# Kernel tuning notes

Measured on AMD Instinct MI355X. Metric: run time of the kernel, lower is better.

## Reference

```python
import jax, jax.numpy as jnp
import numpy as np
import math

EPS = 1e-5  # BatchNorm eps; eval mode with running_mean=0, running_var=1


def maxpool(x, k, p):
    return jax.lax.reduce_window(x, -jnp.inf, jax.lax.max,
                                 (1, 1, k, k), (1, 1, 1, 1),
                                 ((0, 0), (0, 0), (p, p), (p, p)))


def conv1x1(x, w, b=None):
    # x: [B,Cin,H,W], w: [Cout,Cin]
    y = jnp.einsum('oi,bihw->bohw', w, x)
    if b is not None:
        y = y + b[None, :, None, None]
    return y


def bn_eval(x, g, b):
    scale = g / jnp.sqrt(1.0 + EPS)
    return x * scale[None, :, None, None] + b[None, :, None, None]


def setup_inputs() -> dict:
    B, C, H, W = 2, 64, 80, 80
    c1, c2, c3 = 21, 21, 22
    ch = 32  # C//2
    ks = jax.random.split(jax.random.key(0), 16)
    s = 0.05
    inp = {
        'x': jax.random.normal(ks[0], (B, C, H, W), jnp.float32),
        'q1_w': jax.random.normal(ks[1], (c1, c1), jnp.float32) * s,
        'q1_g': jnp.ones((c1,), jnp.float32),
        'q1_b': jnp.zeros((c1,), jnp.float32),
        'q2_w': jax.random.normal(ks[2], (c2, c2), jnp.float32) * s,
        'q2_g': jnp.ones((c2,), jnp.float32),
        'q2_b': jnp.zeros((c2,), jnp.float32),
        'q3_w': jax.random.normal(ks[3], (c3, c3), jnp.float32) * s,
        'q3_g': jnp.ones((c3,), jnp.float32),
        'q3_b': jnp.zeros((c3,), jnp.float32),
        'k_hf_w': jax.random.normal(ks[4], (ch, C), jnp.float32) * s,
        'k_hf_b': jnp.zeros((ch,), jnp.float32),
        'k_lf_w': jax.random.normal(ks[5], (C - ch, C), jnp.float32) * s,
        'k_lf_b': jnp.zeros((C - ch,), jnp.float32),
        'k_fuse_w': jax.random.normal(ks[6], (C, C), jnp.float32) * s,
        'k_fuse_b': jnp.zeros((C,), jnp.float32),
        'v_bn_g': jnp.ones((C,), jnp.float32),
        'v_bn_b': jnp.zeros((C,), jnp.float32),
        'v_w': jax.random.normal(ks[7], (C, C), jnp.float32) * s,
        'v_b': jnp.zeros((C,), jnp.float32),
        'out_w': jax.random.normal(ks[8], (C, C), jnp.float32) * s,
        'out_b': jnp.zeros((C,), jnp.float32),
    }
    return inp


def reference(x, q1_w, q1_g, q1_b, q2_w, q2_g, q2_b, q3_w, q3_g, q3_b,
              k_hf_w, k_hf_b, k_lf_w, k_lf_b, k_fuse_w, k_fuse_b,
              v_bn_g, v_bn_b, v_w, v_b, out_w, out_b):
    B, C, H, W = x.shape
    N = H * W
    c1 = q1_w.shape[0]
    c2 = q2_w.shape[0]
    # Q: ThreeGroupConvQ (split -> 1x1 conv (no bias) -> BN -> ReLU -> concat)
    x1, x2, x3 = jnp.split(x, [c1, c1 + c2], axis=1)
    y1 = jax.nn.relu(bn_eval(conv1x1(x1, q1_w), q1_g, q1_b))
    y2 = jax.nn.relu(bn_eval(conv1x1(x2, q2_w), q2_g, q2_b))
    y3 = jax.nn.relu(bn_eval(conv1x1(x3, q3_w), q3_g, q3_b))
    Q = jnp.concatenate([y1, y2, y3], axis=1)
    # K: ThermalStructureExtractor
    p3 = maxpool(x, 3, 1)
    p5 = maxpool(x, 5, 2)
    low = (p3 + p5) * 0.5
    high = conv1x1(x - low, k_hf_w, k_hf_b)
    lowp = conv1x1(low, k_lf_w, k_lf_b)
    K = conv1x1(jnp.concatenate([high, lowp], axis=1), k_fuse_w, k_fuse_b)
    # V: BN -> 1x1 conv
    V = conv1x1(bn_eval(x, v_bn_g, v_bn_b), v_w, v_b)
    # attention over N = H*W spatial tokens, channel features
    Qc = Q.reshape(B, C, N)
    Kc = K.reshape(B, C, N)
    Vc = V.reshape(B, C, N)
    attn = jax.nn.softmax(
        jnp.einsum('bcn,bcm->bnm', Qc, Kc) / math.sqrt(C), axis=-1)  # [B,N,N]
    out = jnp.einsum('bnm,bcm->bcn', attn, Vc).reshape(B, C, H, W)
    return conv1x1(out, out_w, out_b) + x
```

## Files before the change

### kernel.cpp

```cpp
#include <hip/hip_runtime.h>
#include <hip/hip_bf16.h>


#define BATCH 2
#define CH 64
#define HH 80
#define WW 80
#define NN 6400
#define NT 100
#define KS 5
#define KTPS (NT/KS)
#define EPSV 1e-5f
#define NEGBIG (-1e30f)
#define QP 72
#define LOG2E8 0.18033688f
#define VSP 65

typedef __hip_bfloat16 bf16;
typedef __attribute__((ext_vector_type(8))) short short8;
typedef __attribute__((ext_vector_type(4))) float f4;
#define MFMA16 __builtin_amdgcn_mfma_f32_16x16x32_bf16

__device__ __forceinline__ float b2f(bf16 v){ return __bfloat162float(v); }
__device__ __forceinline__ bf16 f2b(float v){ return __float2bfloat16(v); }
__device__ __forceinline__ float fexp2(float x){
#if __has_builtin(__builtin_amdgcn_exp2f)
  return __builtin_amdgcn_exp2f(x);
#else
  return exp2f(x);
#endif
}

#define OFF_BIAS 0
#define OFF_WH_B 768
#define OFF_LOW_B (768 + 32768)
#define OFF_Q_B   (OFF_LOW_B + BATCH*CH*NN*2)
#define OFF_K_B   (OFF_Q_B   + BATCH*CH*NN*2)
#define OFF_V_B   (OFF_K_B   + BATCH*CH*NN*2)
#define OFF_P_B   (OFF_V_B   + BATCH*CH*NN*2)
#define OFF_ML_B  (OFF_P_B   + BATCH*NT*KS*4096*4)

__global__ __launch_bounds__(256) void setup_fold(
    const float* __restrict__ q1w, const float* __restrict__ q1g, const float* __restrict__ q1b,
    const float* __restrict__ q2w, const float* __restrict__ q2g, const float* __restrict__ q2b,
    const float* __restrict__ q3w, const float* __restrict__ q3g, const float* __restrict__ q3b,
    const float* __restrict__ khw, const float* __restrict__ khb,
    const float* __restrict__ klw, const float* __restrict__ klb,
    const float* __restrict__ kfw, const float* __restrict__ kfb,
    const float* __restrict__ vg,  const float* __restrict__ vbnb,
    const float* __restrict__ vw,  const float* __restrict__ vb,
    float* __restrict__ biasf, bf16* __restrict__ wh)
{
  __shared__ __align__(16) float skf[4096];
  __shared__ __align__(16) float skh[2048];
  __shared__ __align__(16) float skl[2048];

  int tid = threadIdx.x;
  int blk = blockIdx.x;
  #pragma unroll
  for (int i = 0; i < 4; ++i)
    *(float4*)&skf[(i*256 + tid)*4] = *(const float4*)&kfw[(i*256 + tid)*4];
  #pragma unroll
  for (int i = 0; i < 2; ++i) {
    *(float4*)&skh[(i*256 + tid)*4] = *(const float4*)&khw[(i*256 + tid)*4];
    *(float4*)&skl[(i*256 + tid)*4] = *(const float4*)&klw[(i*256 + tid)*4];
  }
  __syncthreads();

  float rs = rsqrtf(1.0f + EPSV);
  bf16* wq   = wh;
  bf16* wvh  = wh + 4096;
  bf16* wa1  = wh + 8192;
  bf16* wa2m = wh + 12288;

  int t = blk*256 + tid;
  int ci = t & 63, co = t >> 6;
  int o = ci*64 + co;

  float w = 0.f, g;
  if (co < 21)      { g = q1g[co];    w = (ci < 21)              ? q1w[co*21 + ci]            : 0.f; }
  else if (co < 42) { g = q2g[co-21]; w = (ci >= 21 && ci < 42)  ? q2w[(co-21)*21 + (ci-21)]  : 0.f; }
  else              { g = q3g[co-42]; w = (ci >= 42)             ? q3w[(co-42)*22 + (ci-42)]  : 0.f; }
  wq[o] = f2b(w * g * rs * LOG2E8);

  float a1 = 0.f, a2 = 0.f;
  #pragma unroll
  for (int j = 0; j < 32; ++j) {
    a1 += skf[co*64 + j]      * skh[j*64 + ci];
    a2 += skf[co*64 + 32 + j] * skl[j*64 + ci];
  }
  wa1[o]  = f2b(a1);
  wa2m[o] = f2b(a2 - a1);
  wvh[o]  = f2b(vw[co*64 + ci] * vg[ci] * rs);

  if (blk == 0 && tid < 64) {
    int c2 = tid;
    float bq;
    if (c2 < 21)      bq = q1b[c2];
    else if (c2 < 42) bq = q2b[c2-21];
    else              bq = q3b[c2-42];
    biasf[c2] = bq * LOG2E8;
    float bk = kfb[c2];
    #pragma unroll
    for (int j = 0; j < 32; ++j) {
      bk += skf[c2*64 + j]      * khb[j];
      bk += skf[c2*64 + 32 + j] * klb[j];
    }
    biasf[64 + c2] = bk;
    float bv = vb[c2];
    for (int ci2 = 0; ci2 < 64; ++ci2) bv += vw[c2*64 + ci2] * vbnb[ci2];
    biasf[128 + c2] = bv;
  }
}

__global__ __launch_bounds__(256) void pool_low(const float* __restrict__ x,
                                                bf16* __restrict__ lowg)
{
  int t4 = (blockIdx.x*256 + threadIdx.x)*4;
  int bc = t4 / NN; int n = t4 % NN;
  int h = n / WW, w0 = n % WW;
  const float* p = x + bc*NN;
  float m5[4], m3[4];
  #pragma unroll
  for (int j=0;j<4;++j){ m5[j]=NEGBIG; m3[j]=NEGBIG; }
  #pragma unroll
  for (int dh = -2; dh <= 2; ++dh) {
    int hh = h + dh; if (hh < 0 || hh >= HH) continue;
    float r[12];
    const float* row = p + hh*WW;
    if (w0 >= 4)      { float4 a = *(const float4*)&row[w0-4]; r[0]=a.x;r[1]=a.y;r[2]=a.z;r[3]=a.w; }
    else              { r[0]=NEGBIG;r[1]=NEGBIG;r[2]=NEGBIG;r[3]=NEGBIG; }
    { float4 a = *(const float4*)&row[w0]; r[4]=a.x;r[5]=a.y;r[6]=a.z;r[7]=a.w; }
    if (w0 + 7 < WW)  { float4 a = *(const float4*)&row[w0+4]; r[8]=a.x;r[9]=a.y;r[10]=a.z;r[11]=a.w; }
    else              { r[8]=NEGBIG;r[9]=NEGBIG;r[10]=NEGBIG;r[11]=NEGBIG; }
    bool in3 = (dh >= -1 && dh <= 1);
    #pragma unroll
    for (int j=0;j<4;++j) {
      float v3 = fmaxf(fmaxf(r[3+j], r[4+j]), r[5+j]);
      float v5 = fmaxf(fmaxf(r[2+j], v3), r[6+j]);
      m5[j] = fmaxf(m5[j], v5);
      if (in3) m3[j] = fmaxf(m3[j], v3);
    }
  }
  ushort4 o;
  o.x = ((__hip_bfloat16_raw)f2b(0.5f*(m3[0]+m5[0]))).x;
  o.y = ((__hip_bfloat16_raw)f2b(0.5f*(m3[1]+m5[1]))).x;
  o.z = ((__hip_bfloat16_raw)f2b(0.5f*(m3[2]+m5[2]))).x;
  o.w = ((__hip_bfloat16_raw)f2b(0.5f*(m3[3]+m5[3]))).x;
  *(ushort4*)&lowg[t4] = o;
}

__global__ __launch_bounds__(256) void qkv_kernel(
    const float* __restrict__ x, const float* __restrict__ biasf,
    const bf16* __restrict__ wh, const bf16* __restrict__ lowg,
    bf16* __restrict__ qgT, bf16* __restrict__ kgT, bf16* __restrict__ vgc)
{
  __shared__ __align__(16) float xs[64*32];
  __shared__ __align__(16) float lows[64*32];
  __shared__ __align__(16) bf16  wbuf[16384];
  __shared__ ushort vs[64*VSP];
  __shared__ float bias[192];

  int tid = threadIdx.x;
  int blk = blockIdx.x;
  int b = blk / (NT*2);
  int rem = blk % (NT*2);
  int tile = rem >> 1, half = rem & 1;
  int n0 = tile*64 + half*32;

  #pragma unroll
  for (int i = 0; i < 8; ++i) {
    int e = i*256 + tid; int c = e >> 5, p = e & 31;
    xs[c*32 + p]   = x[(b*CH + c)*NN + n0 + p];
    lows[c*32 + p] = b2f(lowg[(b*CH + c)*NN + n0 + p]);
  }
  #pragma unroll
  for (int i = 0; i < 16; ++i)
    ((uint2*)wbuf)[i*256 + tid] = ((const uint2*)wh)[i*256 + tid];
  if (tid < 192) bias[tid] = biasf[tid];
  __syncthreads();

  int co = tid & 63, pg = tid >> 6;
  const bf16* wq   = wbuf;
  const bf16* wvh  = wbuf + 4096;
  const bf16* wa1  = wbuf + 8192;
  const bf16* wa2m = wbuf + 12288;

  {
    float bq = bias[co];
    float4 a0 = make_float4(bq,bq,bq,bq), a1v = a0;
    for (int ci = 0; ci < 64; ++ci) {
      float wv = b2f(wq[ci*64 + co]);
      float4 x0 = *(const float4*)&xs[ci*32 + pg*8];
      float4 x1 = *(const float4*)&xs[ci*32 + pg*8 + 4];
      a0.x += wv*x0.x; a0.y += wv*x0.y; a0.z += wv*x0.z; a0.w += wv*x0.w;
      a1v.x += wv*x1.x; a1v.y += wv*x1.y; a1v.z += wv*x1.z; a1v.w += wv*x1.w;
    }
    float q8[8] = {a0.x,a0.y,a0.z,a0.w,a1v.x,a1v.y,a1v.z,a1v.w};
    #pragma unroll
    for (int j=0;j<8;++j)
      qgT[(size_t)(b*NN + n0 + pg*8 + j)*64 + co] = f2b(fmaxf(q8[j], 0.f));
  }
  {
    float bv = bias[128 + co];
    float4 a0 = make_float4(bv,bv,bv,bv), a1v = a0;
    for (int ci = 0; ci < 64; ++ci) {
      float wv = b2f(wvh[ci*64 + co]);
      float4 x0 = *(const float4*)&xs[ci*32 + pg*8];
      float4 x1 = *(const float4*)&xs[ci*32 + pg*8 + 4];
      a0.x += wv*x0.x; a0.y += wv*x0.y; a0.z += wv*x0.z; a0.w += wv*x0.w;
      a1v.x += wv*x1.x; a1v.y += wv*x1.y; a1v.z += wv*x1.z; a1v.w += wv*x1.w;
    }
    float v8[8] = {a0.x,a0.y,a0.z,a0.w,a1v.x,a1v.y,a1v.z,a1v.w};
    #pragma unroll
    for (int j=0;j<8;++j)
      vs[co*VSP + pg*8 + j] = ((__hip_bfloat16_raw)f2b(v8[j])).x;
  }
  __syncthreads();
  {
    int c = tid >> 2, cb = (tid & 3)*8;
    ushort4 o0;
    ushort u[8];
    #pragma unroll
    for (int j=0;j<8;++j) u[j] = vs[c*VSP + cb + j];
    uint4 pk;
    pk.x = (uint)u[0] | ((uint)u[1] << 16);
    pk.y = (uint)u[2] | ((uint)u[3] << 16);
    pk.z = (uint)u[4] | ((uint)u[5] << 16);
    pk.w = (uint)u[6] | ((uint)u[7] << 16);
    *(uint4*)&vgc[(size_t)(b*CH + c)*NN + n0 + cb] = pk;
    (void)o0;
  }
  {
    float bk = bias[64 + co];
    float4 a0 = make_float4(bk,bk,bk,bk), a1v = a0;
    for (int ci = 0; ci < 64; ++ci) {
      float w1 = b2f(wa1[ci*64 + co]);
      float w2 = b2f(wa2m[ci*64 + co]);
      float4 x0 = *(const float4*)&xs[ci*32 + pg*8];
      float4 x1 = *(const float4*)&xs[ci*32 + pg*8 + 4];
      float4 l0 = *(const float4*)&lows[ci*32 + pg*8];
      float4 l1 = *(const float4*)&lows[ci*32 + pg*8 + 4];
      a0.x += w1*x0.x + w2*l0.x; a0.y += w1*x0.y + w2*l0.y;
      a0.z += w1*x0.z + w2*l0.z; a0.w += w1*x0.w + w2*l0.w;
      a1v.x += w1*x1.x + w2*l1.x; a1v.y += w1*x1.y + w2*l1.y;
      a1v.z += w1*x1.z + w2*l1.z; a1v.w += w1*x1.w + w2*l1.w;
    }
    float k8[8] = {a0.x,a0.y,a0.z,a0.w,a1v.x,a1v.y,a1v.z,a1v.w};
    #pragma unroll
    for (int j=0;j<8;++j)
      kgT[(size_t)(b*NN + n0 + pg*8 + j)*64 + co] = f2b(k8[j]);
  }
}

__global__ __launch_bounds__(256) void attn_partial(
    const bf16* __restrict__ qgT, const bf16* __restrict__ kgT, const bf16* __restrict__ vgc,
    float* __restrict__ part, float* __restrict__ pml)
{
  __shared__ __align__(16) char smem[27648];
  bf16* Qld = (bf16*)smem;
  bf16* Pld = (bf16*)smem;
  bf16* Kld = (bf16*)(smem + 9216);
  bf16* Vld = (bf16*)(smem + 18432);

  int tid = threadIdx.x;
  int blk = blockIdx.x;
  int b = blk / (NT*KS);
  int rem = blk % (NT*KS);
  int tile = rem / KS, split = rem % KS;
  int n0 = tile*64;
  int wv = tid >> 6, lane = tid & 63, ln = lane & 15, quad = lane >> 4;
  int arow = (wv*16 + ln)*QP;

  #pragma unroll
  for (int i = 0; i < 4; ++i) {
    int f = (i*256 + tid)*4; int n = f >> 6, c = f & 63;
    *(uint2*)&Qld[n*QP + c] = *(const uint2*)&qgT[(size_t)(b*NN + n0 + n)*64 + c];
  }
  __syncthreads();
  short8 aq0 = *(const short8*)&Qld[arow + quad*8];
  short8 aq1 = *(const short8*)&Qld[arow + 32 + quad*8];

  f4 accO[4];
  float lacc[4];
  #pragma unroll
  for (int t=0;t<4;++t) accO[t] = (f4){0.f,0.f,0.f,0.f};
  #pragma unroll
  for (int r=0;r<4;++r) lacc[r] = 0.f;

  uint2 kreg[4], vreg[4];
  int mbase = split*KTPS*64;
  #pragma unroll
  for (int i = 0; i < 4; ++i) {
    int f = (i*256 + tid)*4; int rr = f >> 6, cc = f & 63;
    kreg[i] = *(const uint2*)&kgT[(size_t)(b*NN + mbase + rr)*64 + cc];
    vreg[i] = *(const uint2*)&vgc[(size_t)(b*CH + rr)*NN + mbase + cc];
  }

  for (int kt = 0; kt < KTPS; ++kt) {
    __syncthreads();
    #pragma unroll
    for (int i = 0; i < 4; ++i) {
      int f = (i*256 + tid)*4; int rr = f >> 6, cc = f & 63;
      *(uint2*)&Kld[rr*QP + cc] = kreg[i];
      *(uint2*)&Vld[rr*QP + cc] = vreg[i];
    }
    __syncthreads();
    if (kt + 1 < KTPS) {
      int m0 = mbase + (kt+1)*64;
      #pragma unroll
      for (int i = 0; i < 4; ++i) {
        int f = (i*256 + tid)*4; int rr = f >> 6, cc = f & 63;
        kreg[i] = *(const uint2*)&kgT[(size_t)(b*NN + m0 + rr)*64 + cc];
        vreg[i] = *(const uint2*)&vgc[(size_t)(b*CH + rr)*NN + m0 + cc];
      }
    }

    f4 accS[4];
    #pragma unroll
    for (int t = 0; t < 4; ++t) {
      short8 bk0 = *(const short8*)&Kld[(t*16+ln)*QP + quad*8];
      short8 bk1 = *(const short8*)&Kld[(t*16+ln)*QP + 32 + quad*8];
      f4 z = (f4){0.f,0.f,0.f,0.f};
      z = MFMA16(aq0, bk0, z, 0, 0, 0);
      accS[t] = MFMA16(aq1, bk1, z, 0, 0, 0);
    }

    #pragma unroll
    for (int r=0;r<4;++r) {
      int n = wv*16 + quad*4 + r;
      #pragma unroll
      for (int t=0;t<4;++t) {
        float p = fexp2(accS[t][r]);
        Pld[n*QP + t*16 + ln] = f2b(p);
        lacc[r] += p;
      }
    }

    short8 ap0 = *(const short8*)&Pld[arow + quad*8];
    short8 ap1 = *(const short8*)&Pld[arow + 32 + quad*8];
    #pragma unroll
    for (int t = 0; t < 4; ++t) {
      short8 bv0 = *(const short8*)&Vld[(t*16+ln)*QP + quad*8];
      short8 bv1 = *(const short8*)&Vld[(t*16+ln)*QP + 32 + quad*8];
      accO[t] = MFMA16(ap0, bv0, accO[t], 0, 0, 0);
      accO[t] = MFMA16(ap1, bv1, accO[t], 0, 0, 0);
    }
  }

  size_t pbase = ((size_t)(b*NT + tile)*KS + split)*4096;
  #pragma unroll
  for (int r=0;r<4;++r) {
    int n = wv*16 + quad*4 + r;
    #pragma unroll
    for (int t=0;t<4;++t)
      part[pbase + n*64 + t*16 + ln] = accO[t][r];
  }
  size_t mlb = ((size_t)(b*NT + tile)*KS + split)*64;
  #pragma unroll
  for (int r=0;r<4;++r) {
    float s = lacc[r];
    s += __shfl_xor(s, 1, 16);
    s += __shfl_xor(s, 2, 16);
    s += __shfl_xor(s, 4, 16);
    s += __shfl_xor(s, 8, 16);
    if (ln == 0) pml[mlb + wv*16 + quad*4 + r] = s;
  }
}

__global__ __launch_bounds__(256) void attn_reduce(
    const float* __restrict__ part, const float* __restrict__ pml,
    const float* __restrict__ x, const float* __restrict__ outw,
    const float* __restrict__ outb, float* __restrict__ out)
{
  __shared__ __align__(16) float Os[32*65];
  __shared__ __align__(16) float Wot[64*65];
  __shared__ float linv[32];

  int tid = threadIdx.x;
  int blk = blockIdx.x;
  int b = blk / (NT*2);
  int rem = blk % (NT*2);
  int tile = rem >> 1, half = rem & 1;
  int nb = half*32;
  size_t base = (size_t)(b*NT + tile)*KS;

  for (int i = 0; i < 16; ++i) {
    int e = i*256 + tid; int co2 = e >> 6, c = e & 63;
    Wot[c*65 + co2] = outw[co2*64 + c];
  }
  if (tid < 32) {
    float l = 0.f;
    #pragma unroll
    for (int s=0;s<KS;++s) l += pml[(base+s)*64 + nb + tid];
    linv[tid] = 1.0f / l;
  }
  __syncthreads();

  #pragma unroll
  for (int i = 0; i < 8; ++i) {
    int e = i*256 + tid; int n = e >> 6, c = e & 63;
    float a = 0.f;
    #pragma unroll
    for (int s=0;s<KS;++s)
      a += part[(base+s)*4096 + (size_t)(nb+n)*64 + c];
    Os[n*65 + c] = a * linv[n];
  }
  __syncthreads();

  {
    int n = tid & 31, cog = tid >> 5;
    float acc[8];
    #pragma unroll
    for (int k=0;k<8;++k) acc[k] = outb[cog*8 + k];
    for (int c = 0; c < 64; ++c) {
      float ov = Os[n*65 + c];
      #pragma unroll
      for (int k=0;k<8;++k) acc[k] += Wot[c*65 + cog*8 + k] * ov;
    }
    #pragma unroll
    for (int k=0;k<8;++k) {
      int co2 = cog*8 + k;
      int idx = (b*CH + co2)*NN + tile*64 + nb + n;
      out[idx] = acc[k] + x[idx];
    }
  }
}

extern "C" void kernel_launch(void* const* d_in, const int* in_sizes, int n_in,
                              void* d_out, int out_size, void* d_ws, size_t ws_size,
                              hipStream_t stream) {
  const float* x    = (const float*)d_in[0];
  const float* q1w  = (const float*)d_in[1];
  const float* q1g  = (const float*)d_in[2];
  const float* q1b  = (const float*)d_in[3];
  const float* q2w  = (const float*)d_in[4];
  const float* q2g  = (const float*)d_in[5];
  const float* q2b  = (const float*)d_in[6];
  const float* q3w  = (const float*)d_in[7];
  const float* q3g  = (const float*)d_in[8];
  const float* q3b  = (const float*)d_in[9];
  const float* khw  = (const float*)d_in[10];
  const float* khb  = (const float*)d_in[11];
  const float* klw  = (const float*)d_in[12];
  const float* klb  = (const float*)d_in[13];
  const float* kfw  = (const float*)d_in[14];
  const float* kfb  = (const float*)d_in[15];
  const float* vbg  = (const float*)d_in[16];
  const float* vbb  = (const float*)d_in[17];
  const float* vw   = (const float*)d_in[18];
  const float* vb   = (const float*)d_in[19];
  const float* outw = (const float*)d_in[20];
  const float* outb = (const float*)d_in[21];

  char*  wsb  = (char*)d_ws;
  float* biasf= (float*)(wsb + OFF_BIAS);
  bf16*  wh   = (bf16*)(wsb + OFF_WH_B);
  bf16*  lowg = (bf16*)(wsb + OFF_LOW_B);
  bf16*  qgT  = (bf16*)(wsb + OFF_Q_B);
  bf16*  kgT  = (bf16*)(wsb + OFF_K_B);
  bf16*  vgc  = (bf16*)(wsb + OFF_V_B);
  float* part = (float*)(wsb + OFF_P_B);
  float* pml  = (float*)(wsb + OFF_ML_B);

  hipLaunchKernelGGL(setup_fold, dim3(16), dim3(256), 0, stream,
                     q1w,q1g,q1b,q2w,q2g,q2b,q3w,q3g,q3b,
                     khw,khb,klw,klb,kfw,kfb,vbg,vbb,vw,vb, biasf, wh);
  hipLaunchKernelGGL(pool_low, dim3(BATCH*CH*NN/1024), dim3(256), 0, stream, x, lowg);
  hipLaunchKernelGGL(qkv_kernel, dim3(BATCH*NT*2), dim3(256), 0, stream,
                     x, biasf, wh, lowg, qgT, kgT, vgc);
  hipLaunchKernelGGL(attn_partial, dim3(BATCH*NT*KS), dim3(256), 0, stream,
                     qgT, kgT, vgc, part, pml);
  hipLaunchKernelGGL(attn_reduce, dim3(BATCH*NT*2), dim3(256), 0, stream,
                     part, pml, x, outw, outb, (float*)d_out);
}
```

Measured before the change: 177.3 us.

## Fuse weight folding, pooling and QKV into one kernel; store attention partials as bf16

Measured after the change: 196.4 us. +10.8%, slower.

```diff
diff --git a/kernel.cpp b/kernel.cpp
--- a/kernel.cpp
+++ b/kernel.cpp
@@ -14,7 +14,6 @@
 #define NEGBIG (-1e30f)
 #define QP 72
 #define LOG2E8 0.18033688f
-#define VSP 65
 
 typedef __hip_bfloat16 bf16;
 typedef __attribute__((ext_vector_type(8))) short short8;
@@ -23,6 +22,10 @@
 
 __device__ __forceinline__ float b2f(bf16 v){ return __bfloat162float(v); }
 __device__ __forceinline__ bf16 f2b(float v){ return __float2bfloat16(v); }
+__device__ __forceinline__ ushort f2bu(float v){ return ((__hip_bfloat16_raw)__float2bfloat16(v)).x; }
+__device__ __forceinline__ float bu2f(ushort u){
+  union { unsigned int i; float f; } w; w.i = ((unsigned int)u) << 16; return w.f;
+}
 __device__ __forceinline__ float fexp2(float x){
 #if __has_builtin(__builtin_amdgcn_exp2f)
   return __builtin_amdgcn_exp2f(x);
@@ -31,16 +34,14 @@
 #endif
 }
 
-#define OFF_BIAS 0
-#define OFF_WH_B 768
-#define OFF_LOW_B (768 + 32768)
-#define OFF_Q_B   (OFF_LOW_B + BATCH*CH*NN*2)
-#define OFF_K_B   (OFF_Q_B   + BATCH*CH*NN*2)
-#define OFF_V_B   (OFF_K_B   + BATCH*CH*NN*2)
-#define OFF_P_B   (OFF_V_B   + BATCH*CH*NN*2)
-#define OFF_ML_B  (OFF_P_B   + BATCH*NT*KS*4096*4)
-
-__global__ __launch_bounds__(256) void setup_fold(
+#define OFF_Q_B   0
+#define OFF_K_B   (OFF_Q_B + BATCH*NN*CH*2)
+#define OFF_V_B   (OFF_K_B + BATCH*NN*CH*2)
+#define OFF_P_B   (OFF_V_B + BATCH*NN*CH*2)
+#define OFF_ML_B  (OFF_P_B + BATCH*NT*KS*4096*2)
+
+__global__ __launch_bounds__(256) void qkv_fused(
+    const float* __restrict__ x,
     const float* __restrict__ q1w, const float* __restrict__ q1g, const float* __restrict__ q1b,
     const float* __restrict__ q2w, const float* __restrict__ q2g, const float* __restrict__ q2b,
     const float* __restrict__ q3w, const float* __restrict__ q3g, const float* __restrict__ q3b,
@@ -49,14 +50,22 @@
     const float* __restrict__ kfw, const float* __restrict__ kfb,
     const float* __restrict__ vg,  const float* __restrict__ vbnb,
     const float* __restrict__ vw,  const float* __restrict__ vb,
-    float* __restrict__ biasf, bf16* __restrict__ wh)
+    bf16* __restrict__ qgT, bf16* __restrict__ kgT, bf16* __restrict__ vgc)
 {
-  __shared__ __align__(16) float skf[4096];
-  __shared__ __align__(16) float skh[2048];
-  __shared__ __align__(16) float skl[2048];
+  __shared__ __align__(16) char sm[86272];
+  float* skf  = (float*)sm;
+  float* skh  = (float*)(sm + 16384);
+  float* skl  = (float*)(sm + 24576);
+  float* xs   = (float*)sm;
+  float* lows = (float*)(sm + 20480);
+  bf16*  wbuf = (bf16*)(sm + 40960);
+  ushort* vs  = (ushort*)(sm + 73728);
+  float* bias = (float*)(sm + 85504);
 
   int tid = threadIdx.x;
   int blk = blockIdx.x;
+  int b = blk / HH, h = blk % HH;
+
   #pragma unroll
   for (int i = 0; i < 4; ++i)
     *(float4*)&skf[(i*256 + tid)*4] = *(const float4*)&kfw[(i*256 + tid)*4];
@@ -68,196 +77,168 @@
   __syncthreads();
 
   float rs = rsqrtf(1.0f + EPSV);
-  bf16* wq   = wh;
-  bf16* wvh  = wh + 4096;
-  bf16* wa1  = wh + 8192;
-  bf16* wa2m = wh + 12288;
-
-  int t = blk*256 + tid;
-  int ci = t & 63, co = t >> 6;
-  int o = ci*64 + co;
-
-  float w = 0.f, g;
-  if (co < 21)      { g = q1g[co];    w = (ci < 21)              ? q1w[co*21 + ci]            : 0.f; }
-  else if (co < 42) { g = q2g[co-21]; w = (ci >= 21 && ci < 42)  ? q2w[(co-21)*21 + (ci-21)]  : 0.f; }
-  else              { g = q3g[co-42]; w = (ci >= 42)             ? q3w[(co-42)*22 + (ci-42)]  : 0.f; }
-  wq[o] = f2b(w * g * rs * LOG2E8);
-
-  float a1 = 0.f, a2 = 0.f;
-  #pragma unroll
-  for (int j = 0; j < 32; ++j) {
-    a1 += skf[co*64 + j]      * skh[j*64 + ci];
-    a2 += skf[co*64 + 32 + j] * skl[j*64 + ci];
-  }
-  wa1[o]  = f2b(a1);
-  wa2m[o] = f2b(a2 - a1);
-  wvh[o]  = f2b(vw[co*64 + ci] * vg[ci] * rs);
-
-  if (blk == 0 && tid < 64) {
+  bf16* wq   = wbuf;
+  bf16* wvh  = wbuf + 4096;
+  bf16* wa1  = wbuf + 8192;
+  bf16* wa2m = wbuf + 12288;
+  #pragma unroll
+  for (int i = 0; i < 16; ++i) {
+    int o = i*256 + tid;
+    int ci = o & 63, co = o >> 6;
+    float w = 0.f, g;
+    if (co < 21)      { g = q1g[co];    w = (ci < 21)             ? q1w[co*21 + ci]           : 0.f; }
+    else if (co < 42) { g = q2g[co-21]; w = (ci >= 21 && ci < 42) ? q2w[(co-21)*21 + (ci-21)] : 0.f; }
+    else              { g = q3g[co-42]; w = (ci >= 42)            ? q3w[(co-42)*22 + (ci-42)] : 0.f; }
+    int o2 = ci*64 + co;
+    wq[o2] = f2b(w * g * rs * LOG2E8);
+    float a1 = 0.f, a2 = 0.f;
+    #pragma unroll
+    for (int j = 0; j < 32; ++j) {
+      a1 += skf[co*64 + j]      * skh[j*64 + ci];
+      a2 += skf[co*64 + 32 + j] * skl[j*64 + ci];
+    }
+    wa1[o2]  = f2b(a1);
+    wa2m[o2] = f2b(a2 - a1);
+    wvh[o2]  = f2b(vw[co*64 + ci] * vg[ci] * rs);
+  }
+  if (tid < 64) {
     int c2 = tid;
     float bq;
     if (c2 < 21)      bq = q1b[c2];
     else if (c2 < 42) bq = q2b[c2-21];
     else              bq = q3b[c2-42];
-    biasf[c2] = bq * LOG2E8;
+    bias[c2] = bq * LOG2E8;
     float bk = kfb[c2];
     #pragma unroll
     for (int j = 0; j < 32; ++j) {
       bk += skf[c2*64 + j]      * khb[j];
       bk += skf[c2*64 + 32 + j] * klb[j];
     }
-    biasf[64 + c2] = bk;
+    bias[64 + c2] = bk;
     float bv = vb[c2];
     for (int ci2 = 0; ci2 < 64; ++ci2) bv += vw[c2*64 + ci2] * vbnb[ci2];
-    biasf[128 + c2] = bv;
-  }
-}
-
-__global__ __launch_bounds__(256) void pool_low(const float* __restrict__ x,
-                                                bf16* __restrict__ lowg)
-{
-  int t4 = (blockIdx.x*256 + threadIdx.x)*4;
-  int bc = t4 / NN; int n = t4 % NN;
-  int h = n / WW, w0 = n % WW;
-  const float* p = x + bc*NN;
-  float m5[4], m3[4];
-  #pragma unroll
-  for (int j=0;j<4;++j){ m5[j]=NEGBIG; m3[j]=NEGBIG; }
-  #pragma unroll
-  for (int dh = -2; dh <= 2; ++dh) {
-    int hh = h + dh; if (hh < 0 || hh >= HH) continue;
-    float r[12];
-    const float* row = p + hh*WW;
-    if (w0 >= 4)      { float4 a = *(const float4*)&row[w0-4]; r[0]=a.x;r[1]=a.y;r[2]=a.z;r[3]=a.w; }
-    else              { r[0]=NEGBIG;r[1]=NEGBIG;r[2]=NEGBIG;r[3]=NEGBIG; }
-    { float4 a = *(const float4*)&row[w0]; r[4]=a.x;r[5]=a.y;r[6]=a.z;r[7]=a.w; }
-    if (w0 + 7 < WW)  { float4 a = *(const float4*)&row[w0+4]; r[8]=a.x;r[9]=a.y;r[10]=a.z;r[11]=a.w; }
-    else              { r[8]=NEGBIG;r[9]=NEGBIG;r[10]=NEGBIG;r[11]=NEGBIG; }
-    bool in3 = (dh >= -1 && dh <= 1);
-    #pragma unroll
-    for (int j=0;j<4;++j) {
-      float v3 = fmaxf(fmaxf(r[3+j], r[4+j]), r[5+j]);
-      float v5 = fmaxf(fmaxf(r[2+j], v3), r[6+j]);
-      m5[j] = fmaxf(m5[j], v5);
-      if (in3) m3[j] = fmaxf(m3[j], v3);
-    }
-  }
-  ushort4 o;
-  o.x = ((__hip_bfloat16_raw)f2b(0.5f*(m3[0]+m5[0]))).x;
-  o.y = ((__hip_bfloat16_raw)f2b(0.5f*(m3[1]+m5[1]))).x;
-  o.z = ((__hip_bfloat16_raw)f2b(0.5f*(m3[2]+m5[2]))).x;
-  o.w = ((__hip_bfloat16_raw)f2b(0.5f*(m3[3]+m5[3]))).x;
-  *(ushort4*)&lowg[t4] = o;
-}
-
-__global__ __launch_bounds__(256) void qkv_kernel(
-    const float* __restrict__ x, const float* __restrict__ biasf,
-    const bf16* __restrict__ wh, const bf16* __restrict__ lowg,
-    bf16* __restrict__ qgT, bf16* __restrict__ kgT, bf16* __restrict__ vgc)
-{
-  __shared__ __align__(16) float xs[64*32];
-  __shared__ __align__(16) float lows[64*32];
-  __shared__ __align__(16) bf16  wbuf[16384];
-  __shared__ ushort vs[64*VSP];
-  __shared__ float bias[192];
-
-  int tid = threadIdx.x;
-  int blk = blockIdx.x;
-  int b = blk / (NT*2);
-  int rem = blk % (NT*2);
-  int tile = rem >> 1, half = rem & 1;
-  int n0 = tile*64 + half*32;
-
-  #pragma unroll
-  for (int i = 0; i < 8; ++i) {
-    int e = i*256 + tid; int c = e >> 5, p = e & 31;
-    xs[c*32 + p]   = x[(b*CH + c)*NN + n0 + p];
-    lows[c*32 + p] = b2f(lowg[(b*CH + c)*NN + n0 + p]);
-  }
-  #pragma unroll
-  for (int i = 0; i < 16; ++i)
-    ((uint2*)wbuf)[i*256 + tid] = ((const uint2*)wh)[i*256 + tid];
-  if (tid < 192) bias[tid] = biasf[tid];
+    bias[128 + c2] = bv;
+  }
+  __syncthreads();
+
+  #pragma unroll
+  for (int i = 0; i < 5; ++i) {
+    int idx4 = (i*256 + tid)*4;
+    int c = idx4 / WW, w0 = idx4 % WW;
+    const float* p = x + (size_t)(b*CH + c)*NN;
+    float m5[4], m3[4];
+    #pragma unroll
+    for (int j=0;j<4;++j){ m5[j]=NEGBIG; m3[j]=NEGBIG; }
+    #pragma unroll
+    for (int dh = -2; dh <= 2; ++dh) {
+      int hh = h + dh; if (hh < 0 || hh >= HH) continue;
+      const float* row = p + hh*WW;
+      float r[12];
+      if (w0 >= 4)      { float4 a = *(const float4*)&row[w0-4]; r[0]=a.x;r[1]=a.y;r[2]=a.z;r[3]=a.w; }
+      else              { r[0]=NEGBIG;r[1]=NEGBIG;r[2]=NEGBIG;r[3]=NEGBIG; }
+      { float4 a = *(const float4*)&row[w0]; r[4]=a.x;r[5]=a.y;r[6]=a.z;r[7]=a.w;
+        if (dh == 0) *(float4*)&xs[c*WW + w0] = a; }
+      if (w0 + 7 < WW)  { float4 a = *(const float4*)&row[w0+4]; r[8]=a.x;r[9]=a.y;r[10]=a.z;r[11]=a.w; }
+      else              { r[8]=NEGBIG;r[9]=NEGBIG;r[10]=NEGBIG;r[11]=NEGBIG; }
+      bool in3 = (dh >= -1 && dh <= 1);
+      #pragma unroll
+      for (int j=0;j<4;++j) {
+        float v3 = fmaxf(fmaxf(r[3+j], r[4+j]), r[5+j]);
+        float v5 = fmaxf(fmaxf(r[2+j], v3), r[6+j]);
+        m5[j] = fmaxf(m5[j], v5);
+        if (in3) m3[j] = fmaxf(m3[j], v3);
+      }
+    }
+    *(float4*)&lows[c*WW + w0] =
+        make_float4(0.5f*(m3[0]+m5[0]), 0.5f*(m3[1]+m5[1]),
+                    0.5f*(m3[2]+m5[2]), 0.5f*(m3[3]+m5[3]));
+  }
   __syncthreads();
 
   int co = tid & 63, pg = tid >> 6;
-  const bf16* wq   = wbuf;
-  const bf16* wvh  = wbuf + 4096;
-  const bf16* wa1  = wbuf + 8192;
-  const bf16* wa2m = wbuf + 12288;
-
+  const float* xr = &xs[pg*20];
+  const float* lr = &lows[pg*20];
   {
     float bq = bias[co];
-    float4 a0 = make_float4(bq,bq,bq,bq), a1v = a0;
+    float a[20];
+    #pragma unroll
+    for (int j=0;j<20;++j) a[j] = bq;
     for (int ci = 0; ci < 64; ++ci) {
       float wv = b2f(wq[ci*64 + co]);
-      float4 x0 = *(const float4*)&xs[ci*32 + pg*8];
-      float4 x1 = *(const float4*)&xs[ci*32 + pg*8 + 4];
-      a0.x += wv*x0.x; a0.y += wv*x0.y; a0.z += wv*x0.z; a0.w += wv*x0.w;
-      a1v.x += wv*x1.x; a1v.y += wv*x1.y; a1v.z += wv*x1.z; a1v.w += wv*x1.w;
-    }
-    float q8[8] = {a0.x,a0.y,a0.z,a0.w,a1v.x,a1v.y,a1v.z,a1v.w};
-    #pragma unroll
-    for (int j=0;j<8;++j)
-      qgT[(size_t)(b*NN + n0 + pg*8 + j)*64 + co] = f2b(fmaxf(q8[j], 0.f));
+      float4 xv[5];
+      #pragma unroll
+      for (int q5=0;q5<5;++q5) xv[q5] = *(const float4*)&xr[ci*WW + q5*4];
+      #pragma unroll
+      for (int q5=0;q5<5;++q5){
+        a[q5*4+0]+=wv*xv[q5].x; a[q5*4+1]+=wv*xv[q5].y;
+        a[q5*4+2]+=wv*xv[q5].z; a[q5*4+3]+=wv*xv[q5].w;
+      }
+    }
+    bf16* dq = qgT + (size_t)(b*NN + h*WW + pg*20)*64 + co;
+    #pragma unroll
+    for (int j=0;j<20;++j) dq[j*64] = f2b(fmaxf(a[j], 0.f));
   }
   {
     float bv = bias[128 + co];
-    float4 a0 = make_float4(bv,bv,bv,bv), a1v = a0;
+    float a[20];
+    #pragma unroll
+    for (int j=0;j<20;++j) a[j] = bv;
     for (int ci = 0; ci < 64; ++ci) {
       float wv = b2f(wvh[ci*64 + co]);
-      float4 x0 = *(const float4*)&xs[ci*32 + pg*8];
-      float4 x1 = *(const float4*)&xs[ci*32 + pg*8 + 4];
-      a0.x += wv*x0.x; a0.y += wv*x0.y; a0.z += wv*x0.z; a0.w += wv*x0.w;
-      a1v.x += wv*x1.x; a1v.y += wv*x1.y; a1v.z += wv*x1.z; a1v.w += wv*x1.w;
-    }
-    float v8[8] = {a0.x,a0.y,a0.z,a0.w,a1v.x,a1v.y,a1v.z,a1v.w};
-    #pragma unroll
-    for (int j=0;j<8;++j)
-      vs[co*VSP + pg*8 + j] = ((__hip_bfloat16_raw)f2b(v8[j])).x;
-  }
-  __syncthreads();
-  {
-    int c = tid >> 2, cb = (tid & 3)*8;
-    ushort4 o0;
-    ushort u[8];
-    #pragma unroll
-    for (int j=0;j<8;++j) u[j] = vs[c*VSP + cb + j];
-    uint4 pk;
-    pk.x = (uint)u[0] | ((uint)u[1] << 16);
-    pk.y = (uint)u[2] | ((uint)u[3] << 16);
-    pk.z = (uint)u[4] | ((uint)u[5] << 16);
-    pk.w = (uint)u[6] | ((uint)u[7] << 16);
-    *(uint4*)&vgc[(size_t)(b*CH + c)*NN + n0 + cb] = pk;
-    (void)o0;
+      float4 xv[5];
+      #pragma unroll
+      for (int q5=0;q5<5;++q5) xv[q5] = *(const float4*)&xr[ci*WW + q5*4];
+      #pragma unroll
+      for (int q5=0;q5<5;++q5){
+        a[q5*4+0]+=wv*xv[q5].x; a[q5*4+1]+=wv*xv[q5].y;
+        a[q5*4+2]+=wv*xv[q5].z; a[q5*4+3]+=wv*xv[q5].w;
+      }
+    }
+    #pragma unroll
+    for (int j=0;j<20;++j) vs[co*88 + pg*20 + j] = f2bu(a[j]);
   }
   {
     float bk = bias[64 + co];
-    float4 a0 = make_float4(bk,bk,bk,bk), a1v = a0;
+    float a[20];
+    #pragma unroll
+    for (int j=0;j<20;++j) a[j] = bk;
     for (int ci = 0; ci < 64; ++ci) {
       float w1 = b2f(wa1[ci*64 + co]);
       float w2 = b2f(wa2m[ci*64 + co]);
-      float4 x0 = *(const float4*)&xs[ci*32 + pg*8];
-      float4 x1 = *(const float4*)&xs[ci*32 + pg*8 + 4];
-      float4 l0 = *(const float4*)&lows[ci*32 + pg*8];
-      float4 l1 = *(const float4*)&lows[ci*32 + pg*8 + 4];
-      a0.x += w1*x0.x + w2*l0.x; a0.y += w1*x0.y + w2*l0.y;
-      a0.z += w1*x0.z + w2*l0.z; a0.w += w1*x0.w + w2*l0.w;
-      a1v.x += w1*x1.x + w2*l1.x; a1v.y += w1*x1.y + w2*l1.y;
-      a1v.z += w1*x1.z + w2*l1.z; a1v.w += w1*x1.w + w2*l1.w;
-    }
-    float k8[8] = {a0.x,a0.y,a0.z,a0.w,a1v.x,a1v.y,a1v.z,a1v.w};
-    #pragma unroll
-    for (int j=0;j<8;++j)
-      kgT[(size_t)(b*NN + n0 + pg*8 + j)*64 + co] = f2b(k8[j]);
+      float4 xv[5], lv[5];
+      #pragma unroll
+      for (int q5=0;q5<5;++q5){
+        xv[q5] = *(const float4*)&xr[ci*WW + q5*4];
+        lv[q5] = *(const float4*)&lr[ci*WW + q5*4];
+      }
+      #pragma unroll
+      for (int q5=0;q5<5;++q5){
+        a[q5*4+0]+=w1*xv[q5].x+w2*lv[q5].x; a[q5*4+1]+=w1*xv[q5].y+w2*lv[q5].y;
+        a[q5*4+2]+=w1*xv[q5].z+w2*lv[q5].z; a[q5*4+3]+=w1*xv[q5].w+w2*lv[q5].w;
+      }
+    }
+    bf16* dk = kgT + (size_t)(b*NN + h*WW + pg*20)*64 + co;
+    #pragma unroll
+    for (int j=0;j<20;++j) dk[j*64] = f2b(a[j]);
+  }
+  __syncthreads();
+  #pragma unroll
+  for (int i = 0; i < 3; ++i) {
+    int idx = i*256 + tid;
+    if (idx < 640) {
+      int c = idx / 10, q = idx % 10;
+      uint4 v = *(const uint4*)&vs[c*88 + q*8];
+      *(uint4*)&vgc[(size_t)(b*CH + c)*NN + h*WW + q*8] = v;
+    }
   }
 }
 
 __global__ __launch_bounds__(256) void attn_partial(
     const bf16* __restrict__ qgT, const bf16* __restrict__ kgT, const bf16* __restrict__ vgc,
-    float* __restrict__ part, float* __restrict__ pml)
+    ushort* __restrict__ part, float* __restrict__ pml)
 {
   __shared__ __align__(16) char smem[27648];
+  __shared__ float lred[256];
   bf16* Qld = (bf16*)smem;
   bf16* Pld = (bf16*)smem;
   bf16* Kld = (bf16*)(smem + 9216);
@@ -278,15 +259,19 @@
     *(uint2*)&Qld[n*QP + c] = *(const uint2*)&qgT[(size_t)(b*NN + n0 + n)*64 + c];
   }
   __syncthreads();
-  short8 aq0 = *(const short8*)&Qld[arow + quad*8];
-  short8 aq1 = *(const short8*)&Qld[arow + 32 + quad*8];
+  short8 bq[4][2];
+  #pragma unroll
+  for (int nt = 0; nt < 4; ++nt) {
+    bq[nt][0] = *(const short8*)&Qld[(nt*16 + ln)*QP + quad*8];
+    bq[nt][1] = *(const short8*)&Qld[(nt*16 + ln)*QP + 32 + quad*8];
+  }
 
   f4 accO[4];
   float lacc[4];
   #pragma unroll
   for (int t=0;t<4;++t) accO[t] = (f4){0.f,0.f,0.f,0.f};
   #pragma unroll
-  for (int r=0;r<4;++r) lacc[r] = 0.f;
+  for (int nt=0;nt<4;++nt) lacc[nt] = 0.f;
 
   uint2 kreg[4], vreg[4];
   int mbase = split*KTPS*64;
@@ -316,26 +301,26 @@
       }
     }
 
+    short8 ak0 = *(const short8*)&Kld[arow + quad*8];
+    short8 ak1 = *(const short8*)&Kld[arow + 32 + quad*8];
     f4 accS[4];
     #pragma unroll
-    for (int t = 0; t < 4; ++t) {
-      short8 bk0 = *(const short8*)&Kld[(t*16+ln)*QP + quad*8];
-      short8 bk1 = *(const short8*)&Kld[(t*16+ln)*QP + 32 + quad*8];
+    for (int nt = 0; nt < 4; ++nt) {
       f4 z = (f4){0.f,0.f,0.f,0.f};
-      z = MFMA16(aq0, bk0, z, 0, 0, 0);
-      accS[t] = MFMA16(aq1, bk1, z, 0, 0, 0);
-    }
-
-    #pragma unroll
-    for (int r=0;r<4;++r) {
-      int n = wv*16 + quad*4 + r;
-      #pragma unroll
-      for (int t=0;t<4;++t) {
-        float p = fexp2(accS[t][r]);
-        Pld[n*QP + t*16 + ln] = f2b(p);
-        lacc[r] += p;
-      }
-    }
+      z = MFMA16(ak0, bq[nt][0], z, 0, 0, 0);
+      accS[nt] = MFMA16(ak1, bq[nt][1], z, 0, 0, 0);
+    }
+    #pragma unroll
+    for (int nt = 0; nt < 4; ++nt) {
+      float p0 = fexp2(accS[nt][0]), p1 = fexp2(accS[nt][1]);
+      float p2 = fexp2(accS[nt][2]), p3 = fexp2(accS[nt][3]);
+      lacc[nt] += (p0 + p1) + (p2 + p3);
+      uint2 pk;
+      pk.x = (uint)f2bu(p0) | ((uint)f2bu(p1) << 16);
+      pk.y = (uint)f2bu(p2) | ((uint)f2bu(p3) << 16);
+      *(uint2*)&Pld[(nt*16 + ln)*QP + wv*16 + quad*4] = pk;
+    }
+    __syncthreads();
 
     short8 ap0 = *(const short8*)&Pld[arow + quad*8];
     short8 ap1 = *(const short8*)&Pld[arow + 32 + quad*8];
@@ -349,27 +334,30 @@
   }
 
   size_t pbase = ((size_t)(b*NT + tile)*KS + split)*4096;
-  #pragma unroll
-  for (int r=0;r<4;++r) {
-    int n = wv*16 + quad*4 + r;
-    #pragma unroll
-    for (int t=0;t<4;++t)
-      part[pbase + n*64 + t*16 + ln] = accO[t][r];
-  }
-  size_t mlb = ((size_t)(b*NT + tile)*KS + split)*64;
-  #pragma unroll
-  for (int r=0;r<4;++r) {
-    float s = lacc[r];
-    s += __shfl_xor(s, 1, 16);
-    s += __shfl_xor(s, 2, 16);
-    s += __shfl_xor(s, 4, 16);
-    s += __shfl_xor(s, 8, 16);
-    if (ln == 0) pml[mlb + wv*16 + quad*4 + r] = s;
+  ushort* pp = part + pbase;
+  #pragma unroll
+  for (int t = 0; t < 4; ++t) {
+    uint2 pk;
+    pk.x = (uint)f2bu(accO[t][0]) | ((uint)f2bu(accO[t][1]) << 16);
+    pk.y = (uint)f2bu(accO[t][2]) | ((uint)f2bu(accO[t][3]) << 16);
+    *(uint2*)&pp[(t*16 + ln)*64 + wv*16 + quad*4] = pk;
+  }
+  #pragma unroll
+  for (int nt = 0; nt < 4; ++nt) {
+    float s = lacc[nt];
+    s += __shfl_xor(s, 16);
+    s += __shfl_xor(s, 32);
+    if (quad == 0) lred[wv*64 + nt*16 + ln] = s;
+  }
+  __syncthreads();
+  if (tid < 64) {
+    size_t mlb = ((size_t)(b*NT + tile)*KS + split)*64;
+    pml[mlb + tid] = (lred[tid] + lred[64 + tid]) + (lred[128 + tid] + lred[192 + tid]);
   }
 }
 
 __global__ __launch_bounds__(256) void attn_reduce(
-    const float* __restrict__ part, const float* __restrict__ pml,
+    const ushort* __restrict__ part, const float* __restrict__ pml,
     const float* __restrict__ x, const float* __restrict__ outw,
     const float* __restrict__ outb, float* __restrict__ out)
 {
@@ -398,13 +386,21 @@
   __syncthreads();
 
   #pragma unroll
-  for (int i = 0; i < 8; ++i) {
-    int e = i*256 + tid; int n = e >> 6, c = e & 63;
-    float a = 0.f;
-    #pragma unroll
-    for (int s=0;s<KS;++s)
-      a += part[(base+s)*4096 + (size_t)(nb+n)*64 + c];
-    Os[n*65 + c] = a * linv[n];
+  for (int j = 0; j < 2; ++j) {
+    int idx = j*256 + tid;
+    int c = idx >> 3, q = idx & 7;
+    float a0=0.f, a1=0.f, a2=0.f, a3=0.f;
+    #pragma unroll
+    for (int s = 0; s < KS; ++s) {
+      uint2 v = *(const uint2*)&part[(base+s)*4096 + (size_t)c*64 + nb + q*4];
+      a0 += bu2f((ushort)(v.x & 0xffff)); a1 += bu2f((ushort)(v.x >> 16));
+      a2 += bu2f((ushort)(v.y & 0xffff)); a3 += bu2f((ushort)(v.y >> 16));
+    }
+    int nl = q*4;
+    Os[(nl+0)*65 + c] = a0 * linv[nl+0];
+    Os[(nl+1)*65 + c] = a1 * linv[nl+1];
+    Os[(nl+2)*65 + c] = a2 * linv[nl+2];
+    Os[(nl+3)*65 + c] = a3 * linv[nl+3];
   }
   __syncthreads();
 
@@ -453,22 +449,17 @@
   const float* outw = (const float*)d_in[20];
   const float* outb = (const float*)d_in[21];
 
-  char*  wsb  = (char*)d_ws;
-  float* biasf= (float*)(wsb + OFF_BIAS);
-  bf16*  wh   = (bf16*)(wsb + OFF_WH_B);
-  bf16*  lowg = (bf16*)(wsb + OFF_LOW_B);
-  bf16*  qgT  = (bf16*)(wsb + OFF_Q_B);
-  bf16*  kgT  = (bf16*)(wsb + OFF_K_B);
-  bf16*  vgc  = (bf16*)(wsb + OFF_V_B);
-  float* part = (float*)(wsb + OFF_P_B);
-  float* pml  = (float*)(wsb + OFF_ML_B);
-
-  hipLaunchKernelGGL(setup_fold, dim3(16), dim3(256), 0, stream,
-                     q1w,q1g,q1b,q2w,q2g,q2b,q3w,q3g,q3b,
-                     khw,khb,klw,klb,kfw,kfb,vbg,vbb,vw,vb, biasf, wh);
-  hipLaunchKernelGGL(pool_low, dim3(BATCH*CH*NN/1024), dim3(256), 0, stream, x, lowg);
-  hipLaunchKernelGGL(qkv_kernel, dim3(BATCH*NT*2), dim3(256), 0, stream,
-                     x, biasf, wh, lowg, qgT, kgT, vgc);
+  char*   wsb  = (char*)d_ws;
+  bf16*   qgT  = (bf16*)(wsb + OFF_Q_B);
+  bf16*   kgT  = (bf16*)(wsb + OFF_K_B);
+  bf16*   vgc  = (bf16*)(wsb + OFF_V_B);
+  ushort* part = (ushort*)(wsb + OFF_P_B);
+  float*  pml  = (float*)(wsb + OFF_ML_B);
+
+  hipLaunchKernelGGL(qkv_fused, dim3(BATCH*HH), dim3(256), 0, stream,
+                     x, q1w,q1g,q1b,q2w,q2g,q2b,q3w,q3g,q3b,
+                     khw,khb,klw,klb,kfw,kfb,vbg,vbb,vw,vb,
+                     qgT, kgT, vgc);
   hipLaunchKernelGGL(attn_partial, dim3(BATCH*NT*KS), dim3(256), 0, stream,
                      qgT, kgT, vgc, part, pml);
   hipLaunchKernelGGL(attn_reduce, dim3(BATCH*NT*2), dim3(256), 0, stream,
```
